# Optimization experiments

Measured on AMD Instinct MI355X. Metric: run time of the kernel, lower is better.

## Reference

```python
import jax, jax.numpy as jnp
import numpy as np

B, T, C, H = 2, 2048, 2048, 16
HD = C // H  # 128 head dim
ROPE_BASE = 10000.0


def setup_inputs() -> dict:
    key = jax.random.key(0)
    k0, k1, k2 = jax.random.split(key, 3)
    x = jax.random.normal(k0, (B, T, C), dtype=jnp.float32)
    W_attn = jax.random.normal(k1, (C, 3 * C), dtype=jnp.float32) * 0.02
    b_attn = jnp.zeros((3 * C,), dtype=jnp.float32)
    W_proj = jax.random.normal(k2, (C, C), dtype=jnp.float32) * 0.02
    b_proj = jnp.zeros((C,), dtype=jnp.float32)
    # freqs_cis = exp(i * t * theta_j), represented as (cos, sin), shape [T, HD//2]
    inv_freq = 1.0 / (ROPE_BASE ** (jnp.arange(0, HD, 2, dtype=jnp.float32) / HD))
    freqs = jnp.outer(jnp.arange(T, dtype=jnp.float32), inv_freq)
    return {"x": x, "W_attn": W_attn, "b_attn": b_attn, "W_proj": W_proj,
            "b_proj": b_proj, "cos": jnp.cos(freqs), "sin": jnp.sin(freqs)}


def _apply_rope(v, cos, sin):
    # v: [B, T, H, HD]; pairs (v[..., 2i], v[..., 2i+1]) rotated by angle freqs[t, i]
    vr = v.reshape(v.shape[:-1] + (-1, 2))
    x0, x1 = vr[..., 0], vr[..., 1]
    c = cos[None, :, None, :]  # [1, T, 1, HD//2]
    s = sin[None, :, None, :]
    o0 = x0 * c - x1 * s
    o1 = x0 * s + x1 * c
    return jnp.stack([o0, o1], axis=-1).reshape(v.shape)


def reference(x, W_attn, b_attn, W_proj, b_proj, cos, sin):
    Bv, Tv, Cv = x.shape
    qkv = x @ W_attn + b_attn                      # [B, T, 3C]
    q, k, v = jnp.split(qkv, 3, axis=-1)
    q = q.reshape(Bv, Tv, H, HD)
    k = k.reshape(Bv, Tv, H, HD)
    v = v.reshape(Bv, Tv, H, HD)
    q = _apply_rope(q, cos, sin)
    k = _apply_rope(k, cos, sin)
    scale = 1.0 / jnp.sqrt(jnp.float32(HD))
    att = jnp.einsum('bqhd,bkhd->bhqk', q, k) * scale
    causal = jnp.tril(jnp.ones((Tv, Tv), dtype=bool))
    att = jnp.where(causal[None, None], att, jnp.finfo(att.dtype).min)
    att = jax.nn.softmax(att, axis=-1)
    y = jnp.einsum('bhqk,bkhd->bqhd', att, v).reshape(Bv, Tv, Cv)
    return y @ W_proj + b_proj
```

## Files before the change

kernel.cpp:

```cpp
#include <hip/hip_runtime.h>

typedef unsigned short u16;
typedef __attribute__((ext_vector_type(8))) short short8;
typedef __attribute__((ext_vector_type(4))) float f32x4;

#define TSEQ 2048
#define NHEAD 16
#define HDIM 128

__device__ __forceinline__ u16 f2bf(float x) {
    unsigned u = __float_as_uint(x);
    return (u16)((u + 0x7fffu + ((u >> 16) & 1u)) >> 16);
}
__device__ __forceinline__ float b2f(u16 h) {
    return __uint_as_float(((unsigned)h) << 16);
}
__device__ __forceinline__ void async16(const void* g, void* l) {
    __builtin_amdgcn_global_load_lds((__attribute__((address_space(1))) void*)(void*)g,
                                     (__attribute__((address_space(3))) void*)l, 16, 0, 0);
}
__device__ __forceinline__ f32x4 zero4() {
    f32x4 z = {0.f, 0.f, 0.f, 0.f};
    return z;
}

template <int CTRL>
__device__ __forceinline__ float dppf(float x) {
    return __int_as_float(__builtin_amdgcn_mov_dpp(__float_as_int(x), CTRL, 0xf, 0xf, true));
}
__device__ __forceinline__ float dpp_max16(float x) {
    x = fmaxf(x, dppf<0xB1>(x));
    x = fmaxf(x, dppf<0x4E>(x));
    x = fmaxf(x, dppf<0x141>(x));
    x = fmaxf(x, dppf<0x140>(x));
    return x;
}
__device__ __forceinline__ float dpp_sum16(float x) {
    x += dppf<0xB1>(x);
    x += dppf<0x4E>(x);
    x += dppf<0x141>(x);
    x += dppf<0x140>(x);
    return x;
}

__global__ void cast_bf16(const float4* __restrict__ in, ushort4* __restrict__ out, int n4) {
    int i = blockIdx.x * 256 + threadIdx.x;
    if (i < n4) {
        float4 v = in[i];
        ushort4 o;
        o.x = f2bf(v.x); o.y = f2bf(v.y); o.z = f2bf(v.z); o.w = f2bf(v.w);
        out[i] = o;
    }
}

__global__ void transpose_cast(const float* __restrict__ in, u16* __restrict__ out, int K, int N) {
    __shared__ float tile[64][65];
    int n0 = blockIdx.x * 64, k0 = blockIdx.y * 64;
    int tx = threadIdx.x & 63, ty = threadIdx.x >> 6;
#pragma unroll
    for (int i = 0; i < 16; i++) {
        int r = ty + i * 4;
        tile[r][tx] = in[(size_t)(k0 + r) * N + n0 + tx];
    }
    __syncthreads();
#pragma unroll
    for (int i = 0; i < 16; i++) {
        int r = ty + i * 4;
        out[(size_t)(n0 + r) * K + k0 + tx] = f2bf(tile[tx][r]);
    }
}

#define WAIT_DS()                                          \
    {                                                      \
        asm volatile("s_waitcnt lgkmcnt(0)" ::: "memory"); \
        __builtin_amdgcn_sched_barrier(0);                 \
    }
#define BAR() __builtin_amdgcn_s_barrier();
#define VBAR_(N)                                               \
    {                                                          \
        asm volatile("s_waitcnt vmcnt(" #N ")" ::: "memory");  \
        __builtin_amdgcn_s_barrier();                          \
    }
#define VBAR(N) VBAR_(N)

#define STAGE(GP, GROW0, LB, KT)                                                                 \
    {                                                                                            \
        const u16* g0__ = (GP) + (size_t)((GROW0) + wave * 16 + grow) * (size_t)K + (KT)*64 +    \
                          gslot * 8;                                                             \
        u16* l0__ = (LB) + wave * 1024;                                                          \
        async16(g0__, l0__);                                                                     \
        async16(g0__ + (size_t)8 * K, l0__ + 512);                                               \
    }

#define LDA4(BASE, MB)                                                              \
    {                                                                               \
        _Pragma("unroll") for (int mm = 0; mm < 4; ++mm) {                          \
            a[mm][0] = *(const short8*)((BASE) + aoff0 + ((MB) + mm) * 1024);       \
            a[mm][1] = *(const short8*)((BASE) + aoff1 + ((MB) + mm) * 1024);       \
        }                                                                           \
    }
#define LDB2(BASE, NB)                                                              \
    {                                                                               \
        _Pragma("unroll") for (int nn = 0; nn < 2; ++nn) {                          \
            b[(NB) + nn][0] = *(const short8*)((BASE) + boff0 + ((NB) + nn) * 1024);\
            b[(NB) + nn][1] = *(const short8*)((BASE) + boff1 + ((NB) + nn) * 1024);\
        }                                                                           \
    }
#define MFQ(MB, NB)                                                                                   \
    {                                                                                                 \
        _Pragma("unroll") for (int mm = 0; mm < 4; ++mm) _Pragma("unroll") for (int nn = 0; nn < 2;   \
                                                                                ++nn) {               \
            acc[(MB) + mm][(NB) + nn] = __builtin_amdgcn_mfma_f32_16x16x32_bf16(                      \
                a[mm][0], b[(NB) + nn][0], acc[(MB) + mm][(NB) + nn], 0, 0, 0);                       \
            acc[(MB) + mm][(NB) + nn] = __builtin_amdgcn_mfma_f32_16x16x32_bf16(                      \
                a[mm][1], b[(NB) + nn][1], acc[(MB) + mm][(NB) + nn], 0, 0, 0);                       \
        }                                                                                             \
    }
#define PRIO_MFQ(MB, NB)                \
    {                                   \
        __builtin_amdgcn_s_setprio(1);  \
        MFQ(MB, NB);                    \
        __builtin_amdgcn_s_setprio(0);  \
    }

__global__ __launch_bounds__(512, 2) void gemm256(
    const u16* __restrict__ A, const u16* __restrict__ Bt, const float* __restrict__ bias,
    u16* __restrict__ qb, u16* __restrict__ kb, u16* __restrict__ vT,
    const float* __restrict__ cosp, const float* __restrict__ sinp,
    int M, int N, int K) {
    extern __shared__ u16 sm[];
    u16* const smA0 = sm;
    u16* const smB0 = sm + 16384;
    u16* const smA1 = sm + 32768;
    u16* const smB1 = sm + 49152;

    const int tid = threadIdx.x;
    const int wave = tid >> 6, lane = tid & 63;
    const int low = lane & 15, quad = lane >> 4;
    const int wr = wave >> 2, wc = wave & 3;
    const int m0 = blockIdx.y * 256, n0 = blockIdx.x * 256;
    const int NT = K >> 6;

    const int grow = lane >> 3;
    const int gslot = (lane & 7) ^ grow;

    const int swz = low & 7;
    const int arow = (wr * 128 + low) * 64;
    const int brow = (wc * 64 + low) * 64;
    const int aoff0 = arow + ((0 + quad) ^ swz) * 8;
    const int aoff1 = arow + ((4 + quad) ^ swz) * 8;
    const int boff0 = brow + ((0 + quad) ^ swz) * 8;
    const int boff1 = brow + ((4 + quad) ^ swz) * 8;

    f32x4 acc[8][4];
#pragma unroll
    for (int i = 0; i < 8; i++)
#pragma unroll
        for (int j = 0; j < 4; j++) acc[i][j] = zero4();
    short8 a[4][2], b[4][2];

    STAGE(A, m0, smA0, 0);
    STAGE(A, m0 + 128, smA0 + 8192, 0);
    STAGE(Bt, n0, smB0, 0);
    STAGE(Bt, n0 + 128, smB0 + 8192, 0);
    STAGE(A, m0, smA1, 1);
    STAGE(A, m0 + 128, smA1 + 8192, 1);
    STAGE(Bt, n0, smB1, 1);
    STAGE(Bt, n0 + 128, smB1 + 8192, 1);
    VBAR(8);

    const int NI = (NT >> 1) - 1;
#pragma unroll 1
    for (int it = 0; it < NI; ++it) {
        const int e = it * 2;
        LDA4(smA0, 0);
        LDB2(smB0, 0);
        LDB2(smB0, 2);
        PRIO_MFQ(0, 0);
        PRIO_MFQ(0, 2);
        LDA4(smA0, 4);
        WAIT_DS();
        BAR();
        PRIO_MFQ(4, 2);
        STAGE(A, m0, smA0, e + 2);
        STAGE(Bt, n0, smB0, e + 2);
        PRIO_MFQ(4, 0);
        VBAR(4);
        LDA4(smA1, 0);
        LDB2(smB1, 0);
        LDB2(smB1, 2);
        STAGE(A, m0 + 128, smA0 + 8192, e + 2);
        STAGE(Bt, n0 + 128, smB0 + 8192, e + 2);
        PRIO_MFQ(0, 0);
        PRIO_MFQ(0, 2);
        LDA4(smA1, 4);
        WAIT_DS();
        BAR();
        PRIO_MFQ(4, 2);
        STAGE(A, m0, smA1, e + 3);
        STAGE(A, m0 + 128, smA1 + 8192, e + 3);
        STAGE(Bt, n0, smB1, e + 3);
        STAGE(Bt, n0 + 128, smB1 + 8192, e + 3);
        PRIO_MFQ(4, 0);
        VBAR(8);
    }
    LDA4(smA0, 0);
    LDB2(smB0, 0);
    LDB2(smB0, 2);
    PRIO_MFQ(0, 0);
    PRIO_MFQ(0, 2);
    LDA4(smA0, 4);
    PRIO_MFQ(4, 2);
    PRIO_MFQ(4, 0);
    VBAR(0);
    LDA4(smA1, 0);
    LDB2(smB1, 0);
    LDB2(smB1, 2);
    PRIO_MFQ(0, 0);
    PRIO_MFQ(0, 2);
    LDA4(smA1, 4);
    PRIO_MFQ(4, 2);
    PRIO_MFQ(4, 0);

    __syncthreads();

    const int which = n0 >> 11;
    const int h0 = (n0 & 2047) >> 7;
    const int bb = m0 >> 11, t0 = m0 & 2047;
    float bvv[4];
#pragma unroll
    for (int nn = 0; nn < 4; ++nn) bvv[nn] = bias[n0 + wc * 64 + nn * 16 + low];

    if (which < 2) {
        u16* dstb = (which == 0 ? qb : kb);
        u16* epi = sm;
#pragma unroll
        for (int hh = 0; hh < 2; ++hh) {
            if ((wc >> 1) == hh) {
#pragma unroll
                for (int mm = 0; mm < 8; ++mm)
#pragma unroll
                    for (int nn = 0; nn < 4; ++nn)
#pragma unroll
                        for (int rr = 0; rr < 4; ++rr)
                            epi[(wr * 128 + mm * 16 + quad * 4 + rr) * 136 +
                                (wc & 1) * 64 + nn * 16 + low] = f2bf(acc[mm][nn][rr] + bvv[nn]);
            }
            __syncthreads();
            {
                const int row = tid >> 1, dh = (tid & 1) * 64;
                const int t = t0 + row;
                u16* dr = dstb + (((size_t)(bb * NHEAD + h0 + hh)) * TSEQ + t) * HDIM + dh;
                u16 vals[64];
#pragma unroll
                for (int qq = 0; qq < 8; ++qq)
                    *(short8*)(vals + qq * 8) = *(const short8*)(epi + row * 136 + dh + qq * 8);
                float csv[32], snv[32];
#pragma unroll
                for (int qq = 0; qq < 8; ++qq) {
                    *(float4*)(csv + qq * 4) =
                        *(const float4*)(cosp + (size_t)t * 64 + (dh >> 1) + qq * 4);
                    *(float4*)(snv + qq * 4) =
                        *(const float4*)(sinp + (size_t)t * 64 + (dh >> 1) + qq * 4);
                }
                u16 ov[64];
#pragma unroll
                for (int pp = 0; pp < 32; ++pp) {
                    float x0 = b2f(vals[2 * pp]), x1 = b2f(vals[2 * pp + 1]);
                    ov[2 * pp] = f2bf(x0 * csv[pp] - x1 * snv[pp]);
                    ov[2 * pp + 1] = f2bf(x0 * snv[pp] + x1 * csv[pp]);
                }
#pragma unroll
                for (int qq = 0; qq < 8; ++qq)
                    *(short8*)(dr + qq * 8) = *(const short8*)(ov + qq * 8);
            }
            __syncthreads();
        }
    } else {
        u16* epi = sm;
#pragma unroll
        for (int hh = 0; hh < 2; ++hh) {
            if ((wc >> 1) == hh) {
#pragma unroll
                for (int mm = 0; mm < 8; ++mm)
#pragma unroll
                    for (int nn = 0; nn < 4; ++nn)
#pragma unroll
                        for (int rr = 0; rr < 4; ++rr)
                            epi[((wc & 1) * 64 + nn * 16 + low) * 264 +
                                wr * 128 + mm * 16 + quad * 4 + rr] = f2bf(acc[mm][nn][rr] + bvv[nn]);
            }
            __syncthreads();
            {
                const int dd = tid >> 2, tc = (tid & 3) * 64;
                u16* dr = vT + ((size_t)(bb * NHEAD + h0 + hh) * HDIM + dd) * TSEQ + t0 + tc;
#pragma unroll
                for (int qq = 0; qq < 8; ++qq)
                    *(short8*)(dr + qq * 8) = *(const short8*)(epi + dd * 264 + tc + qq * 8);
            }
            __syncthreads();
        }
    }
}

#define PMFQ(NB)                                                                                      \
    {                                                                                                 \
        _Pragma("unroll") for (int mm = 0; mm < 4; ++mm) _Pragma("unroll") for (int nn = 0; nn < 2;   \
                                                                                ++nn) {               \
            acc[mm][(NB) + nn] = __builtin_amdgcn_mfma_f32_16x16x32_bf16(                             \
                a[mm][0], b[(NB) + nn][0], acc[mm][(NB) + nn], 0, 0, 0);                              \
            acc[mm][(NB) + nn] = __builtin_amdgcn_mfma_f32_16x16x32_bf16(                             \
                a[mm][1], b[(NB) + nn][1], acc[mm][(NB) + nn], 0, 0, 0);                              \
        }                                                                                             \
    }
#define PPRIO_MFQ(NB)                   \
    {                                   \
        __builtin_amdgcn_s_setprio(1);  \
        PMFQ(NB);                       \
        __builtin_amdgcn_s_setprio(0);  \
    }

__global__ __launch_bounds__(512, 2) void pgemm(
    const u16* __restrict__ A, const u16* __restrict__ Bt, const float* __restrict__ bias,
    float* __restrict__ outf, int M, int N, int K) {
    extern __shared__ u16 sm[];
    u16* const smA0 = sm;
    u16* const smB0 = sm + 8192;
    u16* const smA1 = sm + 24576;
    u16* const smB1 = sm + 32768;

    const int tid = threadIdx.x;
    const int wave = tid >> 6, lane = tid & 63;
    const int low = lane & 15, quad = lane >> 4;
    const int wr = wave >> 2, wc = wave & 3;
    const int m0 = blockIdx.y * 128, n0 = blockIdx.x * 256;
    const int NT = K >> 6;

    const int grow = lane >> 3;
    const int gslot = (lane & 7) ^ grow;

    const int swz = low & 7;
    const int arow = (wr * 64 + low) * 64;
    const int brow = (wc * 64 + low) * 64;
    const int aoff0 = arow + ((0 + quad) ^ swz) * 8;
    const int aoff1 = arow + ((4 + quad) ^ swz) * 8;
    const int boff0 = brow + ((0 + quad) ^ swz) * 8;
    const int boff1 = brow + ((4 + quad) ^ swz) * 8;

    f32x4 acc[4][4];
#pragma unroll
    for (int i = 0; i < 4; i++)
#pragma unroll
        for (int j = 0; j < 4; j++) acc[i][j] = zero4();
    short8 a[4][2], b[4][2];

    STAGE(A, m0, smA0, 0);
    STAGE(Bt, n0, smB0, 0);
    STAGE(Bt, n0 + 128, smB0 + 8192, 0);
    STAGE(A, m0, smA1, 1);
    STAGE(Bt, n0, smB1, 1);
    STAGE(Bt, n0 + 128, smB1 + 8192, 1);
    VBAR(6);

    const int NI = (NT >> 1) - 1;
#pragma unroll 1
    for (int it = 0; it < NI; ++it) {
        const int e = it * 2;
        LDA4(smA0, 0);
        LDB2(smB0, 0);
        LDB2(smB0, 2);
        PPRIO_MFQ(0);
        WAIT_DS();
        BAR();
        STAGE(A, m0, smA0, e + 2);
        STAGE(Bt, n0, smB0, e + 2);
        STAGE(Bt, n0 + 128, smB0 + 8192, e + 2);
        PPRIO_MFQ(2);
        VBAR(6);
        LDA4(smA1, 0);
        LDB2(smB1, 0);
        LDB2(smB1, 2);
        PPRIO_MFQ(0);
        WAIT_DS();
        BAR();
        STAGE(A, m0, smA1, e + 3);
        STAGE(Bt, n0, smB1, e + 3);
        STAGE(Bt, n0 + 128, smB1 + 8192, e + 3);
        PPRIO_MFQ(2);
        VBAR(6);
    }
    LDA4(smA0, 0);
    LDB2(smB0, 0);
    LDB2(smB0, 2);
    PPRIO_MFQ(0);
    PPRIO_MFQ(2);
    VBAR(0);
    LDA4(smA1, 0);
    LDB2(smB1, 0);
    LDB2(smB1, 2);
    PPRIO_MFQ(0);
    PPRIO_MFQ(2);

    float bvv[4];
#pragma unroll
    for (int nn = 0; nn < 4; ++nn) bvv[nn] = bias[n0 + wc * 64 + nn * 16 + low];
#pragma unroll
    for (int mm = 0; mm < 4; ++mm) {
        const int rbase = m0 + wr * 64 + mm * 16 + quad * 4;
#pragma unroll
        for (int nn = 0; nn < 4; ++nn) {
            const int col = n0 + wc * 64 + nn * 16 + low;
#pragma unroll
            for (int r = 0; r < 4; ++r)
                outf[(size_t)(rbase + r) * N + col] = acc[mm][nn][r] + bvv[nn];
        }
    }
}

__global__ __launch_bounds__(256) void flash_attn(const u16* __restrict__ qb, const u16* __restrict__ kb,
                                                  const u16* __restrict__ vT, u16* __restrict__ y) {
    __shared__ u16 Ks[64 * 128];
    __shared__ u16 Vs[128 * 64];
    __shared__ u16 Ps[4][16 * 72];
    const int tid = threadIdx.x;
    const int wave = tid >> 6, lane = tid & 63;
    const int low = lane & 15, quad = lane >> 4;
    const int bh = blockIdx.x;
    const int qt = 31 - blockIdx.y;
    const int q0 = qt * 64 + wave * 16;
    const float scale2 = 0.08838834764831845f * 1.44269504088896f;

    const u16* Qp = qb + ((size_t)bh * TSEQ + q0) * HDIM;
    short8 qf[4];
#pragma unroll
    for (int c = 0; c < 4; c++) qf[c] = *(const short8*)(Qp + (size_t)low * HDIM + c * 32 + quad * 8);

    f32x4 o[8];
#pragma unroll
    for (int d = 0; d < 8; d++) o[d] = zero4();
    float m_i[4], l_i[4];
#pragma unroll
    for (int r = 0; r < 4; r++) { m_i[r] = -1e30f; l_i[r] = 0.f; }

    const u16* Kb = kb + (size_t)bh * TSEQ * HDIM;
    const u16* Vb = vT + (size_t)bh * HDIM * TSEQ;
    u16* Pw = &Ps[wave][0];
    const int ntiles = qt + 1;

    const int krow = tid >> 4, kchunk = tid & 15;
    const int vrow = tid >> 3, vchunk = tid & 7;

    for (int kt = 0; kt < ntiles; ++kt) {
        const int kv0 = kt * 64;
#pragma unroll
        for (int j = 0; j < 4; j++) {
            const int row = j * 16 + krow;
            const int gc = kchunk ^ (row & 7);
            async16(Kb + (size_t)(kv0 + row) * HDIM + gc * 8, Ks + row * 128 + kchunk * 8);
        }
#pragma unroll
        for (int j = 0; j < 4; j++) {
            const int d = j * 32 + vrow;
            const int gc = vchunk ^ (d & 7);
            async16(Vb + (size_t)d * TSEQ + kv0 + gc * 8, Vs + d * 64 + vchunk * 8);
        }
        __syncthreads();

        f32x4 s[4];
#pragma unroll
        for (int h = 0; h < 4; h++) s[h] = zero4();
#pragma unroll
        for (int h = 0; h < 4; h++) {
            const int row = h * 16 + low;
#pragma unroll
            for (int c = 0; c < 4; c++) {
                const int cc = c * 4 + quad;
                short8 kf = *(const short8*)(Ks + row * 128 + (cc ^ (row & 7)) * 8);
                s[h] = __builtin_amdgcn_mfma_f32_16x16x32_bf16(qf[c], kf, s[h], 0, 0, 0);
            }
        }

        float alpha[4];
#pragma unroll
        for (int r = 0; r < 4; r++) {
            const int qg = q0 + quad * 4 + r;
            float sv[4];
#pragma unroll
            for (int h = 0; h < 4; h++)
                sv[h] = (kv0 + h * 16 + low <= qg) ? s[h][r] * scale2 : -1e30f;
            float mx = fmaxf(fmaxf(sv[0], sv[1]), fmaxf(sv[2], sv[3]));
            mx = dpp_max16(mx);
            float mnew = fmaxf(m_i[r], mx);
            alpha[r] = exp2f(m_i[r] - mnew);
            m_i[r] = mnew;
            float p0 = exp2f(sv[0] - mnew);
            float p1 = exp2f(sv[1] - mnew);
            float p2 = exp2f(sv[2] - mnew);
            float p3 = exp2f(sv[3] - mnew);
            float rs = (p0 + p1) + (p2 + p3);
            rs = dpp_sum16(rs);
            l_i[r] = l_i[r] * alpha[r] + rs;
            const int prow = (quad * 4 + r) * 72;
            Pw[prow + low] = f2bf(p0);
            Pw[prow + 16 + low] = f2bf(p1);
            Pw[prow + 32 + low] = f2bf(p2);
            Pw[prow + 48 + low] = f2bf(p3);
        }
        __threadfence_block();

#pragma unroll
        for (int d = 0; d < 8; ++d)
#pragma unroll
            for (int r = 0; r < 4; r++) o[d][r] *= alpha[r];

#pragma unroll
        for (int kc = 0; kc < 2; kc++) {
            short8 pf = *(const short8*)(Pw + low * 72 + kc * 32 + quad * 8);
#pragma unroll
            for (int dd = 0; dd < 8; ++dd) {
                const int vr = dd * 16 + low;
                const int cc = kc * 4 + quad;
                short8 vf = *(const short8*)(Vs + vr * 64 + (cc ^ (vr & 7)) * 8);
                o[dd] = __builtin_amdgcn_mfma_f32_16x16x32_bf16(pf, vf, o[dd], 0, 0, 0);
            }
        }
        __syncthreads();
    }

    const int b = bh >> 4, h = bh & 15;
#pragma unroll
    for (int r = 0; r < 4; r++) {
        float inv = 1.0f / l_i[r];
        size_t row = (size_t)(b * TSEQ + q0 + quad * 4 + r);
        u16* yp = y + row * 2048 + h * HDIM;
#pragma unroll
        for (int d = 0; d < 8; ++d) yp[d * 16 + low] = f2bf(o[d][r] * inv);
    }
}

extern "C" void kernel_launch(void* const* d_in, const int* in_sizes, int n_in,
                              void* d_out, int out_size, void* d_ws, size_t ws_size,
                              hipStream_t stream) {
    const float* x = (const float*)d_in[0];
    const float* Wa = (const float*)d_in[1];
    const float* ba = (const float*)d_in[2];
    const float* Wp = (const float*)d_in[3];
    const float* bp = (const float*)d_in[4];
    const float* cs = (const float*)d_in[5];
    const float* sn = (const float*)d_in[6];
    float* out = (float*)d_out;

    u16* xb = (u16*)d_ws;
    u16* Wab = xb + 8388608;
    u16* Wpb = Wab + 12582912;
    u16* qb = Wpb + 4194304;
    u16* kb = qb + 8388608;
    u16* vT = kb + 8388608;
    u16* y = xb;

    static bool attr_set = false;
    if (!attr_set) {
        hipFuncSetAttribute(reinterpret_cast<const void*>(gemm256),
                            hipFuncAttributeMaxDynamicSharedMemorySize, 131072);
        hipFuncSetAttribute(reinterpret_cast<const void*>(pgemm),
                            hipFuncAttributeMaxDynamicSharedMemorySize, 98304);
        attr_set = true;
    }

    cast_bf16<<<8192, 256, 0, stream>>>((const float4*)x, (ushort4*)xb, 2097152);
    transpose_cast<<<dim3(96, 32), 256, 0, stream>>>(Wa, Wab, 2048, 6144);
    transpose_cast<<<dim3(32, 32), 256, 0, stream>>>(Wp, Wpb, 2048, 2048);
    gemm256<<<dim3(24, 16), 512, 131072, stream>>>(xb, Wab, ba, qb, kb, vT, cs, sn, 4096, 6144, 2048);
    flash_attn<<<dim3(32, 32), 256, 0, stream>>>(qb, kb, vT, y);
    pgemm<<<dim3(8, 32), 512, 98304, stream>>>(y, Wpb, bp, out, 4096, 2048, 2048);
}
```

Before: 395.4 us.

## Double-buffer K/V tiles in flash attention with async prefetch

Converts the flash attention kernel to dynamic shared memory holding two K/V buffers, so the next tile's global-to-LDS loads are issued while the current tile is computed. The single barrier per iteration is replaced with a VBAR wait placed before the prefetch. It also adds s_setprio around the MFMA sections and applies the causal mask only on the diagonal tile. Shared memory grows to about 73 KB per block, which may reduce how many blocks fit per CU, and correctness depends on VBAR waiting for the outstanding async loads and ordering buffer reuse.

```diff
diff --git a/kernel.cpp b/kernel.cpp
--- a/kernel.cpp
+++ b/kernel.cpp
@@ -417,11 +417,29 @@
     }
 }
 
+#define STAGE_KV(KT, SEL)                                                                   \
+    {                                                                                       \
+        const int kv0s = (KT) * 64;                                                         \
+        _Pragma("unroll") for (int j = 0; j < 4; j++) {                                     \
+            const int row = j * 16 + krow;                                                  \
+            const int gc = kchunk ^ (row & 7);                                              \
+            async16(Kb + (size_t)(kv0s + row) * HDIM + gc * 8,                              \
+                    Ksb + (SEL)*8192 + row * 128 + kchunk * 8);                             \
+        }                                                                                   \
+        _Pragma("unroll") for (int j = 0; j < 4; j++) {                                     \
+            const int d = j * 32 + vrow;                                                    \
+            const int gc = vchunk ^ (d & 7);                                                \
+            async16(Vb + (size_t)d * TSEQ + kv0s + gc * 8,                                  \
+                    Vsb + (SEL)*8192 + d * 64 + vchunk * 8);                                \
+        }                                                                                   \
+    }
+
 __global__ __launch_bounds__(256) void flash_attn(const u16* __restrict__ qb, const u16* __restrict__ kb,
                                                   const u16* __restrict__ vT, u16* __restrict__ y) {
-    __shared__ u16 Ks[64 * 128];
-    __shared__ u16 Vs[128 * 64];
-    __shared__ u16 Ps[4][16 * 72];
+    extern __shared__ u16 fsm[];
+    u16* const Ksb = fsm;
+    u16* const Vsb = fsm + 16384;
+    u16* const Psb = fsm + 32768;
     const int tid = threadIdx.x;
     const int wave = tid >> 6, lane = tid & 63;
     const int low = lane & 15, quad = lane >> 4;
@@ -444,41 +462,35 @@
 
     const u16* Kb = kb + (size_t)bh * TSEQ * HDIM;
     const u16* Vb = vT + (size_t)bh * HDIM * TSEQ;
-    u16* Pw = &Ps[wave][0];
+    u16* Pw = Psb + wave * 1152;
     const int ntiles = qt + 1;
 
     const int krow = tid >> 4, kchunk = tid & 15;
     const int vrow = tid >> 3, vchunk = tid & 7;
 
+    STAGE_KV(0, 0);
     for (int kt = 0; kt < ntiles; ++kt) {
         const int kv0 = kt * 64;
-#pragma unroll
-        for (int j = 0; j < 4; j++) {
-            const int row = j * 16 + krow;
-            const int gc = kchunk ^ (row & 7);
-            async16(Kb + (size_t)(kv0 + row) * HDIM + gc * 8, Ks + row * 128 + kchunk * 8);
-        }
-#pragma unroll
-        for (int j = 0; j < 4; j++) {
-            const int d = j * 32 + vrow;
-            const int gc = vchunk ^ (d & 7);
-            async16(Vb + (size_t)d * TSEQ + kv0 + gc * 8, Vs + d * 64 + vchunk * 8);
-        }
-        __syncthreads();
+        VBAR(0);
+        if (kt + 1 < ntiles) STAGE_KV(kt + 1, (kt + 1) & 1);
+        const u16* Kc = Ksb + (kt & 1) * 8192;
+        const u16* Vc = Vsb + (kt & 1) * 8192;
 
         f32x4 s[4];
 #pragma unroll
         for (int h = 0; h < 4; h++) s[h] = zero4();
+        __builtin_amdgcn_s_setprio(1);
 #pragma unroll
         for (int h = 0; h < 4; h++) {
             const int row = h * 16 + low;
 #pragma unroll
             for (int c = 0; c < 4; c++) {
                 const int cc = c * 4 + quad;
-                short8 kf = *(const short8*)(Ks + row * 128 + (cc ^ (row & 7)) * 8);
+                short8 kf = *(const short8*)(Kc + row * 128 + (cc ^ (row & 7)) * 8);
                 s[h] = __builtin_amdgcn_mfma_f32_16x16x32_bf16(qf[c], kf, s[h], 0, 0, 0);
             }
         }
+        __builtin_amdgcn_s_setprio(0);
 
         float alpha[4];
 #pragma unroll
@@ -486,8 +498,12 @@
             const int qg = q0 + quad * 4 + r;
             float sv[4];
 #pragma unroll
-            for (int h = 0; h < 4; h++)
-                sv[h] = (kv0 + h * 16 + low <= qg) ? s[h][r] * scale2 : -1e30f;
+            for (int h = 0; h < 4; h++) sv[h] = s[h][r] * scale2;
+            if (kt == qt) {
+#pragma unroll
+                for (int h = 0; h < 4; h++)
+                    if (kv0 + h * 16 + low > qg) sv[h] = -1e30f;
+            }
             float mx = fmaxf(fmaxf(sv[0], sv[1]), fmaxf(sv[2], sv[3]));
             mx = dpp_max16(mx);
             float mnew = fmaxf(m_i[r], mx);
@@ -513,6 +529,7 @@
 #pragma unroll
             for (int r = 0; r < 4; r++) o[d][r] *= alpha[r];
 
+        __builtin_amdgcn_s_setprio(1);
 #pragma unroll
         for (int kc = 0; kc < 2; kc++) {
             short8 pf = *(const short8*)(Pw + low * 72 + kc * 32 + quad * 8);
@@ -520,11 +537,11 @@
             for (int dd = 0; dd < 8; ++dd) {
                 const int vr = dd * 16 + low;
                 const int cc = kc * 4 + quad;
-                short8 vf = *(const short8*)(Vs + vr * 64 + (cc ^ (vr & 7)) * 8);
+                short8 vf = *(const short8*)(Vc + vr * 64 + (cc ^ (vr & 7)) * 8);
                 o[dd] = __builtin_amdgcn_mfma_f32_16x16x32_bf16(pf, vf, o[dd], 0, 0, 0);
             }
         }
-        __syncthreads();
+        __builtin_amdgcn_s_setprio(0);
     }
 
     const int b = bh >> 4, h = bh & 15;
@@ -564,6 +581,8 @@
                             hipFuncAttributeMaxDynamicSharedMemorySize, 131072);
         hipFuncSetAttribute(reinterpret_cast<const void*>(pgemm),
                             hipFuncAttributeMaxDynamicSharedMemorySize, 98304);
+        hipFuncSetAttribute(reinterpret_cast<const void*>(flash_attn),
+                            hipFuncAttributeMaxDynamicSharedMemorySize, 74752);
         attr_set = true;
     }
 
@@ -571,6 +590,6 @@
     transpose_cast<<<dim3(96, 32), 256, 0, stream>>>(Wa, Wab, 2048, 6144);
     transpose_cast<<<dim3(32, 32), 256, 0, stream>>>(Wp, Wpb, 2048, 2048);
     gemm256<<<dim3(24, 16), 512, 131072, stream>>>(xb, Wab, ba, qb, kb, vT, cs, sn, 4096, 6144, 2048);
-    flash_attn<<<dim3(32, 32), 256, 0, stream>>>(qb, kb, vT, y);
+    flash_attn<<<dim3(32, 32), 256, 74752, stream>>>(qb, kb, vT, y);
     pgemm<<<dim3(8, 32), 512, 98304, stream>>>(y, Wpb, bp, out, 4096, 2048, 2048);
 }
```

After: 399.5 us. About the same (+1.0%).
